# Kernel tuning notes

Hardware: AMD Instinct MI355X
Metric: run time of the kernel (lower is better)

The kernel has to match this reference:

```python
import jax, jax.numpy as jnp
import numpy as np

EPS = 1e-8

def setup_inputs() -> dict:
    key = jax.random.key(0)
    k1, k2, k3, k4 = jax.random.split(key, 4)
    b, in_c, out_c, style_c, k, h, w = 8, 512, 512, 512, 3, 64, 64
    return {
        "input": jax.random.normal(k1, (b, in_c, h, w), dtype=jnp.float32),
        "style": jax.random.normal(k2, (b, style_c), dtype=jnp.float32),
        "w_affine": jax.random.normal(k3, (in_c, style_c), dtype=jnp.float32),  # Linear weight, init N(0,1), runtime-scaled
        "b_affine": jnp.ones((1, in_c), dtype=jnp.float32),                     # Bias init_value=1.0
        "w_conv": jax.random.normal(k4, (out_c, in_c, k, k), dtype=jnp.float32),
    }

def reference(input, style, w_affine, b_affine, w_conv):
    b, in_c, h, w = input.shape
    out_c, _, kh, kw = w_conv.shape
    # Equalized-LR runtime scales (lr_mul=1):
    affine_scale = 1.0 / (w_affine.shape[1] ** 0.5)          # he_std for Linear
    conv_scale = 1.0 / ((in_c * kh * kw) ** 0.5)             # he_std for conv weight
    # affine: Linear + Bias (bias initialized to 1.0)
    s = style @ w_affine.T * affine_scale + b_affine          # [b, in_c]
    # modulate: per-sample weight tensor [b, out_c, in_c, kh, kw]
    wgt = s[:, None, :, None, None] * (w_conv * conv_scale)[None]
    # demodulate
    demod = jax.lax.rsqrt(jnp.sum(wgt * wgt, axis=(2, 3, 4), keepdims=True) + EPS)
    wgt = wgt * demod
    # grouped conv with groups = batch (stride=1, padding=1)
    x = input.reshape(1, b * in_c, h, w)
    wgt = wgt.reshape(b * out_c, in_c, kh, kw)
    out = jax.lax.conv_general_dilated(
        x, wgt,
        window_strides=(1, 1),
        padding=[(1, 1), (1, 1)],
        dimension_numbers=("NCHW", "OIHW", "NCHW"),
        feature_group_count=b,
    )
    return out.reshape(b, out_c, h, w)
```

## Files before the change

### kernel.cpp

```cpp
#include <hip/hip_runtime.h>
#include <hip/hip_bf16.h>

#define BB 8
#define CIN 512
#define COUT 512
#define HH 64
#define WW 64

#define AFF_SCALE 0.044194173824159216f
#define CONV_SCALE 0.014731391274719736f
#define CONV_SCALE2 (1.0f/4608.0f)

typedef short s16x8 __attribute__((ext_vector_type(8)));
typedef float f32x4 __attribute__((ext_vector_type(4)));

__device__ __forceinline__ unsigned short f2bf(float f) {
  __hip_bfloat16 h = __float2bfloat16(f);
  return *reinterpret_cast<unsigned short*>(&h);
}

__global__ __launch_bounds__(256) void affine_kernel(
    const float* __restrict__ style, const float* __restrict__ wa,
    const float* __restrict__ ba, float* __restrict__ smod) {
  int wid  = (blockIdx.x << 2) + (threadIdx.x >> 6);
  int lane = threadIdx.x & 63;
  int b  = wid >> 9;
  int ic = wid & 511;
  const float* s = style + b * CIN;
  const float* w = wa + (size_t)ic * CIN;
  float sum = 0.f;
#pragma unroll
  for (int k = 0; k < CIN / 64; ++k) sum += s[lane + 64 * k] * w[lane + 64 * k];
#pragma unroll
  for (int off = 32; off; off >>= 1) sum += __shfl_down(sum, off, 64);
  if (lane == 0) smod[wid] = sum * AFF_SCALE + ba[ic];
}

__global__ __launch_bounds__(256) void wsq_kernel(
    const float* __restrict__ wc, float* __restrict__ wsq) {
  int i = blockIdx.x * 256 + threadIdx.x;
  const float* p = wc + (size_t)i * 9;
  float s = 0.f;
#pragma unroll
  for (int k = 0; k < 9; ++k) { float v = p[k]; s += v * v; }
  wsq[i] = s;
}

__global__ __launch_bounds__(256) void demod_kernel(
    const float* __restrict__ smod, const float* __restrict__ wsq,
    float* __restrict__ demod) {
  int wid  = (blockIdx.x << 2) + (threadIdx.x >> 6);
  int lane = threadIdx.x & 63;
  int b  = wid >> 9;
  int oc = wid & 511;
  const float* s = smod + b * CIN;
  const float* w = wsq + (size_t)oc * CIN;
  float sum = 0.f;
#pragma unroll
  for (int k = 0; k < CIN / 64; ++k) {
    float sv = s[lane + 64 * k];
    sum += sv * sv * w[lane + 64 * k];
  }
#pragma unroll
  for (int off = 32; off; off >>= 1) sum += __shfl_down(sum, off, 64);
  if (lane == 0) demod[wid] = rsqrtf(sum * CONV_SCALE2 + 1e-8f) * CONV_SCALE;
}

__global__ __launch_bounds__(256) void premod_kernel(
    const float* __restrict__ xin, const float* __restrict__ smod,
    ushort* __restrict__ xt) {
  int n = blockIdx.x * 256 + threadIdx.x;
  int kg = n & 3;
  int x  = (n >> 2) & 63;
  int y  = (n >> 8) & 63;
  int g  = (n >> 14) & 15;
  int b  = n >> 18;
  int ic0 = g * 32 + kg * 8;
  const float* sp = smod + b * CIN + ic0;
  const float* xp = xin + (((size_t)b * CIN + ic0) * HH + y) * WW + x;
  s16x8 o;
#pragma unroll
  for (int j = 0; j < 8; ++j) {
    float v = xp[(size_t)j * HH * WW] * sp[j];
    o[j] = (short)f2bf(v);
  }
  *(s16x8*)(xt + (size_t)n * 8) = o;
}

__global__ __launch_bounds__(256) void wpack_kernel(
    const float* __restrict__ wc, ushort* __restrict__ wfrag) {
  int n = blockIdx.x * 256 + threadIdx.x;
  int l = n & 63;
  int rem = n >> 6;
  int ocg = rem & 31;
  int rem2 = rem >> 5;
  int tap = rem2 % 9;
  int g   = rem2 / 9;
  int oc  = ocg * 16 + (l & 15);
  int ic0 = g * 32 + (l >> 4) * 8;
  int kh = tap / 3, kw = tap - kh * 3;
  s16x8 o;
#pragma unroll
  for (int j = 0; j < 8; ++j) {
    float v = wc[((size_t)oc * CIN + ic0 + j) * 9 + kh * 3 + kw];
    o[j] = (short)f2bf(v);
  }
  *(s16x8*)(wfrag + (size_t)n * 8) = o;
}

#define XS_ROWSZ 4608
#define XS_SIZE  (6 * XS_ROWSZ)
#define WS_SIZE  8192

__global__ __launch_bounds__(256, 2) void conv_mfma(
    const ushort* __restrict__ xt,
    const ushort* __restrict__ wfrag,
    const float* __restrict__ demod,
    float* __restrict__ out) {
  __shared__ char lds[XS_SIZE + 2 * WS_SIZE];
  char* xs  = lds;
  char* ws0 = lds + XS_SIZE;

  int tid = threadIdx.x;
  int l = tid & 63, w = tid >> 6;
  int bid = blockIdx.x;
  int ocb = bid & 3;
  int b   = (bid >> 2) & 7;
  int yt  = bid >> 5;
  int y0  = yt * 4;

  f32x4 acc[8][4];
#pragma unroll
  for (int i = 0; i < 8; ++i)
#pragma unroll
    for (int j = 0; j < 4; ++j) acc[i][j] = f32x4{0.f, 0.f, 0.f, 0.f};

  if (tid < 48) {
    int r = tid >> 3, kgh = (tid >> 1) & 3, side = tid & 1;
    int ct = side ? 65 : 0;
    int off = r * XS_ROWSZ + (ct >> 3) * 512 + kgh * 128 + (ct & 7) * 16;
    *(int4*)(xs + off) = int4{0, 0, 0, 0};
  }
  __syncthreads();

  int sx = tid & 63;
  int skg = w;
  int sct = sx + 1;
  int xs_woff = (sct >> 3) * 512 + skg * 128 + (sct & 7) * 16;

  for (int g = 0; g < 16; ++g) {
    int4 xv[6];
#pragma unroll
    for (int r = 0; r < 6; ++r) {
      int gy = y0 - 1 + r;
      int4 t = {0, 0, 0, 0};
      if (gy >= 0 && gy < HH)
        t = *(const int4*)(xt + ((((size_t)(b * 16 + g) * 4096) + gy * 64 + sx) * 32 + skg * 8));
      xv[r] = t;
    }
    int4 wv0, wv1;
    {
      const int4* wsrc = (const int4*)(wfrag + ((size_t)(g * 9 + 0) * 32 + ocb * 8) * 512);
      wv0 = wsrc[tid];
      wv1 = wsrc[tid + 256];
    }
#pragma unroll
    for (int r = 0; r < 6; ++r) *(int4*)(xs + r * XS_ROWSZ + xs_woff) = xv[r];
    *(int4*)(ws0 + tid * 16) = wv0;
    *(int4*)(ws0 + tid * 16 + 4096) = wv1;
    __syncthreads();

#pragma unroll
    for (int tap = 0; tap < 9; ++tap) {
      char* wscur = ws0 + (tap & 1) * WS_SIZE;
      int4 nv0, nv1;
      if (tap < 8) {
        const int4* wsrc = (const int4*)(wfrag + ((size_t)(g * 9 + tap + 1) * 32 + ocb * 8) * 512);
        nv0 = wsrc[tid];
        nv1 = wsrc[tid + 256];
      }
      const int dy = tap / 3 - 1, dx = tap % 3 - 1;
      const int rb = w + 1 + dy;
      s16x8 bfr[4];
#pragma unroll
      for (int fn = 0; fn < 4; ++fn) {
        int c2 = fn * 16 + (l & 15) + dx + 1;
        bfr[fn] = *(const s16x8*)(xs + rb * XS_ROWSZ + (c2 >> 3) * 512 + (l >> 4) * 128 + (c2 & 7) * 16);
      }
#pragma unroll
      for (int fm = 0; fm < 8; ++fm) {
        s16x8 afr = *(const s16x8*)(wscur + fm * 1024 + l * 16);
#pragma unroll
        for (int fn = 0; fn < 4; ++fn)
          acc[fm][fn] = __builtin_amdgcn_mfma_f32_16x16x32_bf16(afr, bfr[fn], acc[fm][fn], 0, 0, 0);
      }
      if (tap < 8) {
        char* wsnxt = ws0 + ((tap + 1) & 1) * WS_SIZE;
        *(int4*)(wsnxt + tid * 16) = nv0;
        *(int4*)(wsnxt + tid * 16 + 4096) = nv1;
      }
      __syncthreads();
    }
  }

  int oc_base = ocb * 128;
  int gy = y0 + w;
#pragma unroll
  for (int fm = 0; fm < 8; ++fm) {
#pragma unroll
    for (int r = 0; r < 4; ++r) {
      int oc = oc_base + fm * 16 + (l >> 4) * 4 + r;
      float dm = demod[b * COUT + oc];
#pragma unroll
      for (int fn = 0; fn < 4; ++fn) {
        out[(((size_t)b * COUT + oc) * 4096) + gy * 64 + fn * 16 + (l & 15)] =
            acc[fm][fn][r] * dm;
      }
    }
  }
}

extern "C" void kernel_launch(void* const* d_in, const int* in_sizes, int n_in,
                              void* d_out, int out_size, void* d_ws, size_t ws_size,
                              hipStream_t stream) {
  const float* input = (const float*)d_in[0];
  const float* style = (const float*)d_in[1];
  const float* wa    = (const float*)d_in[2];
  const float* ba    = (const float*)d_in[3];
  const float* wconv = (const float*)d_in[4];
  float* out = (float*)d_out;

  float* smod  = (float*)d_ws;
  float* demod = smod + BB * CIN;
  float* wsq   = demod + BB * COUT;
  ushort* wfrag = (ushort*)(wsq + (size_t)COUT * CIN);
  ushort* xt    = wfrag + (size_t)16 * 9 * 32 * 64 * 8;

  affine_kernel<<<BB * CIN / 4, 256, 0, stream>>>(style, wa, ba, smod);
  wsq_kernel<<<COUT * CIN / 256, 256, 0, stream>>>(wconv, wsq);
  demod_kernel<<<BB * COUT / 4, 256, 0, stream>>>(smod, wsq, demod);
  wpack_kernel<<<16 * 9 * 32 * 64 / 256, 256, 0, stream>>>(wconv, wfrag);
  premod_kernel<<<BB * 16 * 64 * 64 * 4 / 256, 256, 0, stream>>>(input, smod, xt);
  conv_mfma<<<BB * 4 * 16, 256, 0, stream>>>(xt, wfrag, demod, out);
}
```

Before: 163.9 us.

## Double-buffer input tile in LDS and prefetch next group during taps

Adds a second LDS buffer for the input tile so the next channel group's rows are loaded from global memory at tap 0 and written to the alternate buffer at tap 8. This hides global input load latency behind MFMA work and removes the extra per-group barrier. It also raises wave priority around the MFMA loop and replaces __syncthreads with an explicit lgkmcnt wait plus s_barrier under sched_barriers. The larger LDS footprint (about 87KB per block) and extra held registers may reduce occupancy below the 2 blocks per CU requested by launch bounds.

```diff
diff --git a/kernel.cpp b/kernel.cpp
--- a/kernel.cpp
+++ b/kernel.cpp
@@ -117,9 +117,8 @@
     const ushort* __restrict__ wfrag,
     const float* __restrict__ demod,
     float* __restrict__ out) {
-  __shared__ char lds[XS_SIZE + 2 * WS_SIZE];
-  char* xs  = lds;
-  char* ws0 = lds + XS_SIZE;
+  __shared__ char lds[2 * XS_SIZE + 2 * WS_SIZE];
+  char* wsb = lds + 2 * XS_SIZE;
 
   int tid = threadIdx.x;
   int l = tid & 63, w = tid >> 6;
@@ -135,71 +134,97 @@
 #pragma unroll
     for (int j = 0; j < 4; ++j) acc[i][j] = f32x4{0.f, 0.f, 0.f, 0.f};
 
-  if (tid < 48) {
-    int r = tid >> 3, kgh = (tid >> 1) & 3, side = tid & 1;
-    int ct = side ? 65 : 0;
-    int off = r * XS_ROWSZ + (ct >> 3) * 512 + kgh * 128 + (ct & 7) * 16;
-    *(int4*)(xs + off) = int4{0, 0, 0, 0};
-  }
-  __syncthreads();
+  if (tid < 96) {
+    int r    = tid >> 4;
+    int kg   = (tid >> 2) & 3;
+    int side = (tid >> 1) & 1;
+    int buf  = tid & 1;
+    int ct   = side ? 65 : 0;
+    int off  = buf * XS_SIZE + r * XS_ROWSZ + (ct >> 3) * 512 + kg * 128 + (ct & 7) * 16;
+    *(int4*)(lds + off) = int4{0, 0, 0, 0};
+  }
 
   int sx = tid & 63;
   int skg = w;
   int sct = sx + 1;
   int xs_woff = (sct >> 3) * 512 + skg * 128 + (sct & 7) * 16;
 
-  for (int g = 0; g < 16; ++g) {
-    int4 xv[6];
+  {
+    const int4* wsrc = (const int4*)(wfrag + (size_t)(ocb * 8) * 512);
+    int4 wv0 = wsrc[tid];
+    int4 wv1 = wsrc[tid + 256];
 #pragma unroll
     for (int r = 0; r < 6; ++r) {
       int gy = y0 - 1 + r;
       int4 t = {0, 0, 0, 0};
       if (gy >= 0 && gy < HH)
-        t = *(const int4*)(xt + ((((size_t)(b * 16 + g) * 4096) + gy * 64 + sx) * 32 + skg * 8));
-      xv[r] = t;
+        t = *(const int4*)(xt + ((((size_t)(b * 16 + 0) * 4096) + gy * 64 + sx) * 32 + skg * 8));
+      *(int4*)(lds + r * XS_ROWSZ + xs_woff) = t;
     }
-    int4 wv0, wv1;
-    {
-      const int4* wsrc = (const int4*)(wfrag + ((size_t)(g * 9 + 0) * 32 + ocb * 8) * 512);
-      wv0 = wsrc[tid];
-      wv1 = wsrc[tid + 256];
-    }
-#pragma unroll
-    for (int r = 0; r < 6; ++r) *(int4*)(xs + r * XS_ROWSZ + xs_woff) = xv[r];
-    *(int4*)(ws0 + tid * 16) = wv0;
-    *(int4*)(ws0 + tid * 16 + 4096) = wv1;
-    __syncthreads();
-
+    *(int4*)(wsb + tid * 16) = wv0;
+    *(int4*)(wsb + tid * 16 + 4096) = wv1;
+  }
+  __syncthreads();
+
+  int4 xv[6];
+  for (int g = 0; g < 16; ++g) {
+    char* xs_r = lds + (g & 1) * XS_SIZE;
+    char* xs_w = lds + ((g & 1) ^ 1) * XS_SIZE;
 #pragma unroll
     for (int tap = 0; tap < 9; ++tap) {
-      char* wscur = ws0 + (tap & 1) * WS_SIZE;
+      const int k = g * 9 + tap;
+      char* ws_cur = wsb + (k & 1) * WS_SIZE;
+      char* ws_nxt = wsb + ((k & 1) ^ 1) * WS_SIZE;
+
+      if (tap == 0 && g < 15) {
+#pragma unroll
+        for (int r = 0; r < 6; ++r) {
+          int gy = y0 - 1 + r;
+          xv[r] = int4{0, 0, 0, 0};
+          if (gy >= 0 && gy < HH)
+            xv[r] = *(const int4*)(xt + ((((size_t)(b * 16 + g + 1) * 4096) + gy * 64 + sx) * 32 + skg * 8));
+        }
+      }
       int4 nv0, nv1;
-      if (tap < 8) {
-        const int4* wsrc = (const int4*)(wfrag + ((size_t)(g * 9 + tap + 1) * 32 + ocb * 8) * 512);
+      if (k < 143) {
+        const int4* wsrc = (const int4*)(wfrag + ((size_t)(k + 1) * 32 + ocb * 8) * 512);
         nv0 = wsrc[tid];
         nv1 = wsrc[tid + 256];
       }
+
       const int dy = tap / 3 - 1, dx = tap % 3 - 1;
       const int rb = w + 1 + dy;
       s16x8 bfr[4];
 #pragma unroll
       for (int fn = 0; fn < 4; ++fn) {
         int c2 = fn * 16 + (l & 15) + dx + 1;
-        bfr[fn] = *(const s16x8*)(xs + rb * XS_ROWSZ + (c2 >> 3) * 512 + (l >> 4) * 128 + (c2 & 7) * 16);
-      }
+        bfr[fn] = *(const s16x8*)(xs_r + rb * XS_ROWSZ + (c2 >> 3) * 512 + (l >> 4) * 128 + (c2 & 7) * 16);
+      }
+
+      __builtin_amdgcn_s_setprio(1);
 #pragma unroll
       for (int fm = 0; fm < 8; ++fm) {
-        s16x8 afr = *(const s16x8*)(wscur + fm * 1024 + l * 16);
+        s16x8 afr = *(const s16x8*)(ws_cur + fm * 1024 + l * 16);
 #pragma unroll
         for (int fn = 0; fn < 4; ++fn)
           acc[fm][fn] = __builtin_amdgcn_mfma_f32_16x16x32_bf16(afr, bfr[fn], acc[fm][fn], 0, 0, 0);
       }
-      if (tap < 8) {
-        char* wsnxt = ws0 + ((tap + 1) & 1) * WS_SIZE;
-        *(int4*)(wsnxt + tid * 16) = nv0;
-        *(int4*)(wsnxt + tid * 16 + 4096) = nv1;
-      }
-      __syncthreads();
+      __builtin_amdgcn_s_setprio(0);
+
+      if (k < 143) {
+        *(int4*)(ws_nxt + tid * 16) = nv0;
+        *(int4*)(ws_nxt + tid * 16 + 4096) = nv1;
+      }
+      if (tap == 8 && g < 15) {
+#pragma unroll
+        for (int r = 0; r < 6; ++r)
+          *(int4*)(xs_w + r * XS_ROWSZ + xs_woff) = xv[r];
+      }
+
+      asm volatile("s_waitcnt lgkmcnt(0)" ::: "memory");
+      __builtin_amdgcn_sched_barrier(0);
+      __builtin_amdgcn_s_barrier();
+      __builtin_amdgcn_sched_barrier(0);
     }
   }
 
```

New measurement: 156.6 us. 4.4% less time.
